# Kernel tuning notes

Hardware: AMD Instinct MI355X
Metric: run time of the kernel (lower is better)

## Reference

```python
import jax, jax.numpy as jnp
import numpy as np

EMBED_DIM = 256
NUM_HEADS = 8
TEMPERATURE = 10000.0
SCALE = 100.0
EPS = 1e-5


def setup_inputs() -> dict:
    key = jax.random.key(0)
    k1, k2, k3 = jax.random.split(key, 3)
    B, N, H, Wd = 1, 300, 24, 80
    # depths in a realistic positive range
    predict_depth = jax.random.uniform(k1, (B, N), dtype=jnp.float32) * 60.0
    depth_map = jax.random.uniform(k2, (B, H, Wd), dtype=jnp.float32) * 60.0
    # nn.Linear(embed_dim, num_heads): store as (in, out)
    W = jax.random.normal(k3, (EMBED_DIM, NUM_HEADS), dtype=jnp.float32) * 0.05
    b = jnp.zeros((NUM_HEADS,), dtype=jnp.float32)
    return {"predict_depth": predict_depth, "depth_map": depth_map, "W": W, "b": b}


def reference(predict_depth, depth_map, W, b):
    B, H, Wd = depth_map.shape
    HW = H * Wd
    N = predict_depth.shape[1]
    dm = depth_map.reshape(B, HW)
    pd = jax.nn.relu(predict_depth)
    # depth log-ratio: (B, N, HW)
    delta = jnp.log((pd[:, :, None] + EPS) / (dm[:, None, :] + EPS))
    # sine/cos embedding with interleaved sin/cos per frequency -> (B, N, HW, 256)
    dim_t = TEMPERATURE ** (jnp.arange(EMBED_DIM // 2, dtype=jnp.float32) * 2.0 / EMBED_DIM)
    pos = delta[..., None] * SCALE / dim_t  # (B, N, HW, 128)
    pos = jnp.stack((jnp.sin(pos), jnp.cos(pos)), axis=-1).reshape(B, N, HW, EMBED_DIM)
    # computed under torch.no_grad() in the original
    pos = jax.lax.stop_gradient(pos)
    # Linear(256 -> num_heads) + ReLU
    out = jax.nn.relu(pos @ W + b)  # (B, N, HW, heads)
    # permute(0,3,1,2).flatten(0,1) -> (B*heads, N, HW)
    out = jnp.transpose(out, (0, 3, 1, 2)).reshape(B * NUM_HEADS, N, HW)
    return out
```

## Files before the change

kernel.cpp:

```cpp
#include <hip/hip_runtime.h>
#include <hip/hip_bf16.h>

#define NPTS   300
#define HW_SZ  1920
#define NH     8
#define TOTAL  (NPTS * HW_SZ)
#define K      256
#define NCOL   2400
#define L2T128 0.10381025293350249f

#define BM  128
#define BN  64
#define BK  64
#define LDK 72
#define SNP 132

typedef __attribute__((ext_vector_type(8))) short short8;
typedef __attribute__((ext_vector_type(4))) float floatx4;

__device__ __forceinline__ unsigned bf16_rne(float x) {
    unsigned u = __float_as_uint(x);
    return (u + 0x7fffu + ((u >> 16) & 1u)) >> 16;
}

__global__ __launch_bounds__(256) void dre_fused(const float* __restrict__ pd,
                                                 const float* __restrict__ dm,
                                                 const float* __restrict__ W,
                                                 const float* __restrict__ b,
                                                 float* __restrict__ out)
{
    __shared__ float kf[128];
    __shared__ float ldm[BM];
    __shared__ float sn[8 * SNP];
    __shared__ float cn[8 * SNP];
    __shared__ float wl[2048];
    __shared__ unsigned short As[BM * LDK];
    __shared__ unsigned short Bs[BN * LDK];

    const int tid  = threadIdx.x;
    const int m0   = blockIdx.x * BM;
    const int c0   = blockIdx.y * BN;
    const int n0   = c0 >> 3;

    if (tid < 128) {
        kf[tid] = 100.0f * exp2f(-(float)tid * L2T128);
    } else {
        ldm[tid - 128] = __logf(dm[m0 + tid - 128] + 1e-5f);
    }
    {
        const float4* Wv = (const float4*)W;
        *(float4*)&wl[tid * 8]     = Wv[tid * 2];
        *(float4*)&wl[tid * 8 + 4] = Wv[tid * 2 + 1];
    }
    __syncthreads();

    {
        const int nl = tid >> 5;
        const int nn = n0 + nl;
        const float pv = (nn < NPTS) ? pd[nn] : 0.0f;
        const float lp = __logf(fmaxf(pv, 0.0f) + 1e-5f);
#pragma unroll
        for (int j = 0; j < 4; ++j) {
            const int i = (tid & 31) * 4 + j;
            const float a = kf[i] * lp;
            sn[nl * SNP + i] = __sinf(a);
            cn[nl * SNP + i] = __cosf(a);
        }
    }

    const int w    = tid >> 6;
    const int lane = tid & 63;
    const int quad = lane >> 4;
    const int l16  = lane & 15;

    floatx4 acc[2][4];
#pragma unroll
    for (int mi = 0; mi < 2; ++mi)
#pragma unroll
        for (int nf = 0; nf < 4; ++nf) acc[mi][nf] = (floatx4){0.f, 0.f, 0.f, 0.f};

    const int arow = tid >> 1;
    const int akb  = (tid & 1) * 32;
    const int bc   = tid & 63;
    const int bnl  = bc >> 3;
    const int bh   = bc & 7;
    const int bkb  = (tid >> 6) * 16;

    __syncthreads();

    for (int k0 = 0; k0 < K; k0 += BK) {
        const bool isSin = (k0 >= 128);
        const int  ibase = k0 & 64;

        {
            const float ld = ldm[arow];
            uint4 u[4];
            unsigned* uw = (unsigned*)u;
#pragma unroll
            for (int g = 0; g < 16; ++g) {
                const int i = ibase + akb + g * 2;
                const float a0 = kf[i] * ld;
                const float a1 = kf[i + 1] * ld;
                const float v0 = isSin ? __sinf(a0) : __cosf(a0);
                const float v1 = isSin ? __sinf(a1) : __cosf(a1);
                uw[g] = bf16_rne(v0) | (bf16_rne(v1) << 16);
            }
#pragma unroll
            for (int g = 0; g < 4; ++g)
                *(uint4*)&As[arow * LDK + akb + g * 8] = u[g];
        }
        {
            uint4 u[2];
            unsigned* uw = (unsigned*)u;
#pragma unroll
            for (int g = 0; g < 8; ++g) {
                const int i = ibase + bkb + g * 2;
                const float s0 = sn[bnl * SNP + i],     c0v = cn[bnl * SNP + i];
                const float s1 = sn[bnl * SNP + i + 1], c1v = cn[bnl * SNP + i + 1];
                const float ws0 = wl[i * 16 + bh],        wc0 = wl[i * 16 + 8 + bh];
                const float ws1 = wl[(i + 1) * 16 + bh],  wc1 = wl[(i + 1) * 16 + 8 + bh];
                const float v0 = isSin ? (wc0 * s0 - ws0 * c0v) : (ws0 * s0 + wc0 * c0v);
                const float v1 = isSin ? (wc1 * s1 - ws1 * c1v) : (ws1 * s1 + wc1 * c1v);
                uw[g] = bf16_rne(v0) | (bf16_rne(v1) << 16);
            }
            *(uint4*)&Bs[bc * LDK + bkb]     = u[0];
            *(uint4*)&Bs[bc * LDK + bkb + 8] = u[1];
        }
        __syncthreads();

#pragma unroll
        for (int ks = 0; ks < 2; ++ks) {
            const int koff = ks * 32 + quad * 8;
            short8 a0 = *(const short8*)(&As[(w * 32 + l16) * LDK + koff]);
            short8 a1 = *(const short8*)(&As[(w * 32 + 16 + l16) * LDK + koff]);
#pragma unroll
            for (int nf = 0; nf < 4; ++nf) {
                short8 bb = *(const short8*)(&Bs[(nf * 16 + l16) * LDK + koff]);
                acc[0][nf] = __builtin_amdgcn_mfma_f32_16x16x32_bf16(a0, bb, acc[0][nf], 0, 0, 0);
                acc[1][nf] = __builtin_amdgcn_mfma_f32_16x16x32_bf16(a1, bb, acc[1][nf], 0, 0, 0);
            }
        }
        __syncthreads();
    }

    const float bias = b[lane & 7];
#pragma unroll
    for (int mi = 0; mi < 2; ++mi) {
#pragma unroll
        for (int nf = 0; nf < 4; ++nf) {
            const int c = c0 + nf * 16 + l16;
            if (c < NCOL) {
                const int n = c >> 3, h = c & 7;
                const int hw = m0 + w * 32 + mi * 16 + quad * 4;
                floatx4 v = acc[mi][nf];
                v.x = fmaxf(v.x + bias, 0.0f);
                v.y = fmaxf(v.y + bias, 0.0f);
                v.z = fmaxf(v.z + bias, 0.0f);
                v.w = fmaxf(v.w + bias, 0.0f);
                *(floatx4*)(out + (size_t)h * TOTAL + (size_t)n * HW_SZ + hw) = v;
            }
        }
    }
}

extern "C" void kernel_launch(void* const* d_in, const int* in_sizes, int n_in,
                              void* d_out, int out_size, void* d_ws, size_t ws_size,
                              hipStream_t stream) {
    const float* pd = (const float*)d_in[0];
    const float* dm = (const float*)d_in[1];
    const float* W  = (const float*)d_in[2];
    const float* b  = (const float*)d_in[3];
    float* out = (float*)d_out;

    dre_fused<<<dim3(HW_SZ / BM, (NCOL + BN - 1) / BN), 256, 0, stream>>>(pd, dm, W, b, out);
}
```

Baseline: 80.44 us.

## Widen N tile to 128 and reuse sincos results across sin/cos K chunks

The column tile doubles from 64 to 128, so each block computes the A-side (depth-map) trig values once for twice as many output columns. A single sincos call now produces both cos and sin, and the sin half is stashed in registers for the later K chunks instead of being recomputed. The K loop is fully unrolled, the sn/cn padding changes, and launch bounds now request 2 blocks per CU. The price is more accumulator and stash registers, which may limit occupancy, and fewer blocks in the grid (15x19), which lowers parallelism.

```diff
diff --git a/kernel.cpp b/kernel.cpp
--- a/kernel.cpp
+++ b/kernel.cpp
@@ -5,15 +5,15 @@
 #define HW_SZ  1920
 #define NH     8
 #define TOTAL  (NPTS * HW_SZ)
-#define K      256
 #define NCOL   2400
 #define L2T128 0.10381025293350249f
 
 #define BM  128
-#define BN  64
-#define BK  64
+#define BN  128
 #define LDK 72
-#define SNP 132
+#define SNP 129
+#define MT  (HW_SZ / BM)
+#define CT  19
 
 typedef __attribute__((ext_vector_type(8))) short short8;
 typedef __attribute__((ext_vector_type(4))) float floatx4;
@@ -23,30 +23,27 @@
     return (u + 0x7fffu + ((u >> 16) & 1u)) >> 16;
 }
 
-__global__ __launch_bounds__(256) void dre_fused(const float* __restrict__ pd,
-                                                 const float* __restrict__ dm,
-                                                 const float* __restrict__ W,
-                                                 const float* __restrict__ b,
-                                                 float* __restrict__ out)
+__global__ __launch_bounds__(256, 2) void dre_fused2(const float* __restrict__ pd,
+                                                     const float* __restrict__ dm,
+                                                     const float* __restrict__ W,
+                                                     const float* __restrict__ b,
+                                                     float* __restrict__ out)
 {
     __shared__ float kf[128];
     __shared__ float ldm[BM];
-    __shared__ float sn[8 * SNP];
-    __shared__ float cn[8 * SNP];
+    __shared__ float sn[16 * SNP];
+    __shared__ float cn[16 * SNP];
     __shared__ float wl[2048];
     __shared__ unsigned short As[BM * LDK];
     __shared__ unsigned short Bs[BN * LDK];
 
-    const int tid  = threadIdx.x;
-    const int m0   = blockIdx.x * BM;
-    const int c0   = blockIdx.y * BN;
-    const int n0   = c0 >> 3;
+    const int tid = threadIdx.x;
+    const int m0  = blockIdx.x * BM;
+    const int c0  = blockIdx.y * BN;
+    const int n0  = c0 >> 3;
 
-    if (tid < 128) {
-        kf[tid] = 100.0f * exp2f(-(float)tid * L2T128);
-    } else {
-        ldm[tid - 128] = __logf(dm[m0 + tid - 128] + 1e-5f);
-    }
+    if (tid < 128) kf[tid] = 100.0f * exp2f(-(float)tid * L2T128);
+    else           ldm[tid - 128] = __logf(dm[m0 + tid - 128] + 1e-5f);
     {
         const float4* Wv = (const float4*)W;
         *(float4*)&wl[tid * 8]     = Wv[tid * 2];
@@ -55,16 +52,17 @@
     __syncthreads();
 
     {
-        const int nl = tid >> 5;
+        const int nl = tid >> 4;
         const int nn = n0 + nl;
         const float pv = (nn < NPTS) ? pd[nn] : 0.0f;
         const float lp = __logf(fmaxf(pv, 0.0f) + 1e-5f);
 #pragma unroll
-        for (int j = 0; j < 4; ++j) {
-            const int i = (tid & 31) * 4 + j;
-            const float a = kf[i] * lp;
-            sn[nl * SNP + i] = __sinf(a);
-            cn[nl * SNP + i] = __cosf(a);
+        for (int j = 0; j < 8; ++j) {
+            const int i = (tid & 15) * 8 + j;
+            float s, c;
+            __sincosf(kf[i] * lp, &s, &c);
+            sn[nl * SNP + i] = s;
+            cn[nl * SNP + i] = c;
         }
     }
 
@@ -73,58 +71,67 @@
     const int quad = lane >> 4;
     const int l16  = lane & 15;
 
-    floatx4 acc[2][4];
+    const int arow = tid >> 1;
+    const int akb  = (tid & 1) * 32;
+    const int bc   = tid & 127;
+    const int bnl  = bc >> 3;
+    const int bh   = bc & 7;
+    const int bkb  = (tid >> 7) * 32;
+
+    floatx4 acc[2][8];
 #pragma unroll
     for (int mi = 0; mi < 2; ++mi)
 #pragma unroll
-        for (int nf = 0; nf < 4; ++nf) acc[mi][nf] = (floatx4){0.f, 0.f, 0.f, 0.f};
+        for (int nf = 0; nf < 8; ++nf) acc[mi][nf] = (floatx4){0.f, 0.f, 0.f, 0.f};
 
-    const int arow = tid >> 1;
-    const int akb  = (tid & 1) * 32;
-    const int bc   = tid & 63;
-    const int bnl  = bc >> 3;
-    const int bh   = bc & 7;
-    const int bkb  = (tid >> 6) * 16;
+    unsigned stash[2][16];
 
     __syncthreads();
 
-    for (int k0 = 0; k0 < K; k0 += BK) {
-        const bool isSin = (k0 >= 128);
-        const int  ibase = k0 & 64;
-
-        {
+#pragma unroll
+    for (int ch = 0; ch < 4; ++ch) {
+        const int ibase = (ch & 1) * 64;
+        if (ch < 2) {
             const float ld = ldm[arow];
-            uint4 u[4];
-            unsigned* uw = (unsigned*)u;
+            unsigned uc[16];
 #pragma unroll
             for (int g = 0; g < 16; ++g) {
-                const int i = ibase + akb + g * 2;
-                const float a0 = kf[i] * ld;
-                const float a1 = kf[i + 1] * ld;
-                const float v0 = isSin ? __sinf(a0) : __cosf(a0);
-                const float v1 = isSin ? __sinf(a1) : __cosf(a1);
-                uw[g] = bf16_rne(v0) | (bf16_rne(v1) << 16);
+                const int i = ibase + akb + 2 * g;
+                float s0, c0v, s1, c1v;
+                __sincosf(kf[i] * ld,     &s0, &c0v);
+                __sincosf(kf[i + 1] * ld, &s1, &c1v);
+                uc[g]        = bf16_rne(c0v) | (bf16_rne(c1v) << 16);
+                stash[ch][g] = bf16_rne(s0)  | (bf16_rne(s1)  << 16);
             }
 #pragma unroll
-            for (int g = 0; g < 4; ++g)
-                *(uint4*)&As[arow * LDK + akb + g * 8] = u[g];
+            for (int g4 = 0; g4 < 4; ++g4)
+                *(uint4*)&As[arow * LDK + akb + g4 * 8] =
+                    make_uint4(uc[g4*4], uc[g4*4+1], uc[g4*4+2], uc[g4*4+3]);
+        } else {
+#pragma unroll
+            for (int g4 = 0; g4 < 4; ++g4)
+                *(uint4*)&As[arow * LDK + akb + g4 * 8] =
+                    make_uint4(stash[ch-2][g4*4],   stash[ch-2][g4*4+1],
+                               stash[ch-2][g4*4+2], stash[ch-2][g4*4+3]);
         }
         {
-            uint4 u[2];
-            unsigned* uw = (unsigned*)u;
+            unsigned uq[16];
 #pragma unroll
-            for (int g = 0; g < 8; ++g) {
-                const int i = ibase + bkb + g * 2;
-                const float s0 = sn[bnl * SNP + i],     c0v = cn[bnl * SNP + i];
-                const float s1 = sn[bnl * SNP + i + 1], c1v = cn[bnl * SNP + i + 1];
-                const float ws0 = wl[i * 16 + bh],        wc0 = wl[i * 16 + 8 + bh];
-                const float ws1 = wl[(i + 1) * 16 + bh],  wc1 = wl[(i + 1) * 16 + 8 + bh];
-                const float v0 = isSin ? (wc0 * s0 - ws0 * c0v) : (ws0 * s0 + wc0 * c0v);
-                const float v1 = isSin ? (wc1 * s1 - ws1 * c1v) : (ws1 * s1 + wc1 * c1v);
-                uw[g] = bf16_rne(v0) | (bf16_rne(v1) << 16);
+            for (int g = 0; g < 16; ++g) {
+                const int i = ibase + bkb + 2 * g;
+                const float s0  = sn[bnl * SNP + i],     cc0 = cn[bnl * SNP + i];
+                const float s1  = sn[bnl * SNP + i + 1], cc1 = cn[bnl * SNP + i + 1];
+                const float ws0 = wl[i * 16 + bh],       wc0 = wl[i * 16 + 8 + bh];
+                const float ws1 = wl[(i+1) * 16 + bh],   wc1 = wl[(i+1) * 16 + 8 + bh];
+                float v0, v1;
+                if (ch < 2) { v0 = ws0*s0 + wc0*cc0; v1 = ws1*s1 + wc1*cc1; }
+                else        { v0 = wc0*s0 - ws0*cc0; v1 = wc1*s1 - ws1*cc1; }
+                uq[g] = bf16_rne(v0) | (bf16_rne(v1) << 16);
             }
-            *(uint4*)&Bs[bc * LDK + bkb]     = u[0];
-            *(uint4*)&Bs[bc * LDK + bkb + 8] = u[1];
+#pragma unroll
+            for (int g4 = 0; g4 < 4; ++g4)
+                *(uint4*)&Bs[bc * LDK + bkb + g4 * 8] =
+                    make_uint4(uq[g4*4], uq[g4*4+1], uq[g4*4+2], uq[g4*4+3]);
         }
         __syncthreads();
 
@@ -134,7 +141,7 @@
             short8 a0 = *(const short8*)(&As[(w * 32 + l16) * LDK + koff]);
             short8 a1 = *(const short8*)(&As[(w * 32 + 16 + l16) * LDK + koff]);
 #pragma unroll
-            for (int nf = 0; nf < 4; ++nf) {
+            for (int nf = 0; nf < 8; ++nf) {
                 short8 bb = *(const short8*)(&Bs[(nf * 16 + l16) * LDK + koff]);
                 acc[0][nf] = __builtin_amdgcn_mfma_f32_16x16x32_bf16(a0, bb, acc[0][nf], 0, 0, 0);
                 acc[1][nf] = __builtin_amdgcn_mfma_f32_16x16x32_bf16(a1, bb, acc[1][nf], 0, 0, 0);
@@ -147,7 +154,7 @@
 #pragma unroll
     for (int mi = 0; mi < 2; ++mi) {
 #pragma unroll
-        for (int nf = 0; nf < 4; ++nf) {
+        for (int nf = 0; nf < 8; ++nf) {
             const int c = c0 + nf * 16 + l16;
             if (c < NCOL) {
                 const int n = c >> 3, h = c & 7;
@@ -172,5 +179,5 @@
     const float* b  = (const float*)d_in[3];
     float* out = (float*)d_out;
 
-    dre_fused<<<dim3(HW_SZ / BM, (NCOL + BN - 1) / BN), 256, 0, stream>>>(pd, dm, W, b, out);
+    dre_fused2<<<dim3(MT, CT), 256, 0, stream>>>(pd, dm, W, b, out);
 }
```

Result: no change. 79.52 us (-1.1%).
